# Kernel optimization log

Measured on AMD Instinct MI355X. Metric: run time of the kernel, lower is better.

The kernel has to match this reference:

```python
import jax, jax.numpy as jnp
import numpy as np

B, S, D, E, F, TOP_K = 4, 2048, 1024, 8, 4096, 2

def setup_inputs() -> dict:
    key = jax.random.key(0)
    ks = jax.random.split(key, 7)
    sd = 1.0 / np.sqrt(D)
    sf = 1.0 / np.sqrt(F)
    return {
        "x": jax.random.normal(ks[0], (B, S, D), dtype=jnp.float32),
        "gate_w": jax.random.normal(ks[1], (D, E), dtype=jnp.float32) * sd,
        "gate_b": jnp.zeros((E,), dtype=jnp.float32),
        "w1": jax.random.normal(ks[2], (E, D, F), dtype=jnp.float32) * sd,
        "b1": jnp.zeros((E, F), dtype=jnp.float32),
        "w2": jax.random.normal(ks[3], (E, F, D), dtype=jnp.float32) * sf,
        "b2": jnp.zeros((E, D), dtype=jnp.float32),
    }

def reference(x, gate_w, gate_b, w1, b1, w2, b2):
    # Gating: softmax over experts, take top-k, renormalize top-k weights.
    logits = jnp.einsum("bsd,de->bse", x, gate_w) + gate_b
    probs = jax.nn.softmax(logits, axis=-1)
    topw, topi = jax.lax.top_k(probs, TOP_K)            # [B,S,K]
    topw = topw / jnp.sum(topw, axis=-1, keepdims=True)
    # Sparse combine weights as dense [B,S,E] (zero for non-selected experts).
    combine = jnp.sum(jax.nn.one_hot(topi, E, dtype=x.dtype) * topw[..., None], axis=-2)  # [B,S,E]
    # Expert FFN (Linear -> ReLU -> Linear) computed for all experts, combined sparsely.
    mid = jax.nn.relu(jnp.einsum("bsd,edf->bsef", x, w1) + b1)   # [B,S,E,F]
    out_e = jnp.einsum("bsef,efd->bsed", mid, w2) + b2           # [B,S,E,D]
    return jnp.einsum("bsed,bse->bsd", out_e, combine)
```

## Files before the change

kernel.cpp:

```cpp
#include <hip/hip_runtime.h>

#define B_ 4
#define S_ 2048
#define T_ (B_*S_)
#define D_ 1024
#define E_ 8
#define F_ 4096
#define K_ 2
#define TK_ (T_*K_)

typedef __attribute__((ext_vector_type(8))) short short8;
typedef __attribute__((ext_vector_type(4))) float f32x4;

__device__ __forceinline__ unsigned short bf16rn(float f) {
    unsigned int u = __builtin_bit_cast(unsigned int, f);
    u = u + 0x7FFFu + ((u >> 16) & 1u);
    return (unsigned short)(u >> 16);
}
__device__ __forceinline__ float bf16tof(unsigned short h) {
    unsigned int u = ((unsigned int)h) << 16;
    return __builtin_bit_cast(float, u);
}

#define GLOAD16(gp, lp) __builtin_amdgcn_global_load_lds( \
    (const __attribute__((address_space(1))) unsigned int*)(gp), \
    (__attribute__((address_space(3))) unsigned int*)(lp), 16, 0, 0)

__global__ void gate_kernel(const float* __restrict__ x, const float* __restrict__ gw,
                            const float* __restrict__ gb, int* __restrict__ topi,
                            float* __restrict__ topw, int* __restrict__ counts)
{
    const int gid  = blockIdx.x * blockDim.x + threadIdx.x;
    const int t    = gid >> 6;
    const int lane = threadIdx.x & 63;
    if (t >= T_) return;
    const float* xr = x + (size_t)t * D_;
    float p[E_];
#pragma unroll
    for (int e = 0; e < E_; ++e) p[e] = 0.f;
    for (int j = 0; j < D_ / 64; ++j) {
        const int d = j * 64 + lane;
        const float xv = xr[d];
        const float* g = gw + (size_t)d * E_;
#pragma unroll
        for (int e = 0; e < E_; ++e) p[e] += xv * g[e];
    }
#pragma unroll
    for (int off = 32; off > 0; off >>= 1) {
#pragma unroll
        for (int e = 0; e < E_; ++e) p[e] += __shfl_xor(p[e], off);
    }
    if (lane == 0) {
#pragma unroll
        for (int e = 0; e < E_; ++e) p[e] += gb[e];
        float m = p[0];
#pragma unroll
        for (int e = 1; e < E_; ++e) m = fmaxf(m, p[e]);
        float ex[E_];
#pragma unroll
        for (int e = 0; e < E_; ++e) ex[e] = expf(p[e] - m);
        int i0 = 0; float v0 = ex[0];
#pragma unroll
        for (int e = 1; e < E_; ++e) if (ex[e] > v0) { v0 = ex[e]; i0 = e; }
        int i1 = -1; float v1 = -1.f;
#pragma unroll
        for (int e = 0; e < E_; ++e) if (e != i0 && ex[e] > v1) { v1 = ex[e]; i1 = e; }
        const float inv = 1.f / (v0 + v1);
        topi[t*2]   = i0; topi[t*2+1] = i1;
        topw[t*2]   = v0 * inv; topw[t*2+1] = v1 * inv;
        atomicAdd(&counts[i0], 1);
        atomicAdd(&counts[i1], 1);
    }
}

__global__ void offsets_kernel(const int* __restrict__ counts, int* __restrict__ offsets,
                               int* __restrict__ cursor)
{
    if (threadIdx.x == 0 && blockIdx.x == 0) {
        int acc = 0;
        for (int e = 0; e < E_; ++e) { offsets[e] = acc; cursor[e] = acc; acc += counts[e]; }
    }
}

__global__ void scatter_kernel(const int* __restrict__ topi, const float* __restrict__ topw,
                               int* __restrict__ cursor, int* __restrict__ list_token,
                               float* __restrict__ list_w, int* __restrict__ slot_of)
{
    const int t = blockIdx.x * blockDim.x + threadIdx.x;
    if (t >= T_) return;
#pragma unroll
    for (int k = 0; k < K_; ++k) {
        const int e = topi[t*2 + k];
        const int s = atomicAdd(&cursor[e], 1);
        list_token[s] = t;
        list_w[s]     = topw[t*2 + k];
        slot_of[t*2 + k] = s;
    }
}

__global__ void convert_x_kernel(const float* __restrict__ x,
                                 unsigned short* __restrict__ xh,
                                 unsigned short* __restrict__ xl)
{
    const size_t i = (size_t)blockIdx.x * blockDim.x + threadIdx.x;
    const float4 v = ((const float4*)x)[i];
    ushort4 h, l;
    h.x = bf16rn(v.x); l.x = bf16rn(v.x - bf16tof(h.x));
    h.y = bf16rn(v.y); l.y = bf16rn(v.y - bf16tof(h.y));
    h.z = bf16rn(v.z); l.z = bf16rn(v.z - bf16tof(h.z));
    h.w = bf16rn(v.w); l.w = bf16rn(v.w - bf16tof(h.w));
    ((ushort4*)xh)[i] = h;
    ((ushort4*)xl)[i] = l;
}

__global__ __launch_bounds__(256) void tconv_kernel(const float* __restrict__ in,
                                                    unsigned short* __restrict__ oh,
                                                    unsigned short* __restrict__ ol,
                                                    int R, int C)
{
    const int e = blockIdx.z;
    const size_t eb = (size_t)e * R * C;
    const int c0 = blockIdx.x * 32, r0 = blockIdx.y * 32;
    __shared__ float t[32][33];
    const int tx = threadIdx.x & 31, ty = threadIdx.x >> 5;
#pragma unroll
    for (int p = 0; p < 4; ++p)
        t[ty + 8*p][tx] = in[eb + (size_t)(r0 + ty + 8*p) * C + c0 + tx];
    __syncthreads();
#pragma unroll
    for (int p = 0; p < 4; ++p) {
        const float v = t[tx][ty + 8*p];
        const unsigned short h = bf16rn(v);
        const unsigned short lo = bf16rn(v - bf16tof(h));
        const size_t o = eb + (size_t)(c0 + ty + 8*p) * R + r0 + tx;
        oh[o] = h; ol[o] = lo;
    }
}

__global__ __launch_bounds__(256, 2) void gemm1_mfma(
    const unsigned short* __restrict__ xh, const unsigned short* __restrict__ xl,
    const unsigned short* __restrict__ w1h, const unsigned short* __restrict__ w1l,
    const float* __restrict__ b1,
    const int* __restrict__ list_token, const int* __restrict__ offsets,
    const int* __restrict__ counts,
    unsigned short* __restrict__ midh, unsigned short* __restrict__ midl,
    int f0, int Fc)
{
    const int e   = blockIdx.z;
    const int cnt = counts[e];
    const int r0  = blockIdx.x * 128;
    if (r0 >= cnt) return;
    const int base = offsets[e];
    const int fcol = f0 + blockIdx.y * 128;

    __shared__ unsigned short lds[4 * 4096];

    const int tid = threadIdx.x;
    const int w = tid >> 6, l = tid & 63;

    const unsigned short* gsrc[8];
    {
        const unsigned short* Abase = (w == 0) ? xh : xl;
        const unsigned short* Bbase = (w == 2) ? w1h : w1l;
        const int jr = l >> 2, pos = l & 3;
#pragma unroll
        for (int j = 0; j < 8; ++j) {
            const int r  = j * 16 + jr;
            const int kg = pos ^ ((r >> 1) & 3);
            if (w < 2) {
                int idx = base + r0 + r; if (idx > TK_ - 1) idx = TK_ - 1;
                const int tok = list_token[idx];
                gsrc[j] = Abase + (size_t)tok * D_ + kg * 8;
            } else {
                gsrc[j] = Bbase + ((size_t)e * F_ + fcol + r) * D_ + kg * 8;
            }
        }
    }
    unsigned short* ldst[8];
#pragma unroll
    for (int j = 0; j < 8; ++j) ldst[j] = &lds[w * 4096 + j * 512];

    const int wr = w >> 1, wc = w & 1;
    int idxA[4], idxB[4];
#pragma unroll
    for (int m = 0; m < 4; ++m) {
        const int row = wr * 64 + m * 16 + (l & 15);
        const int kgr = (l >> 4) ^ ((row >> 1) & 3);
        idxA[m] = row * 32 + kgr * 8;
    }
#pragma unroll
    for (int n = 0; n < 4; ++n) {
        const int row = wc * 64 + n * 16 + (l & 15);
        const int kgr = (l >> 4) ^ ((row >> 1) & 3);
        idxB[n] = row * 32 + kgr * 8;
    }

    f32x4 acc[4][4];
#pragma unroll
    for (int m = 0; m < 4; ++m)
#pragma unroll
        for (int n = 0; n < 4; ++n) { f32x4 z = {0.f,0.f,0.f,0.f}; acc[m][n] = z; }

    for (int k0 = 0; k0 < D_; k0 += 32) {
#pragma unroll
        for (int j = 0; j < 8; ++j) GLOAD16(gsrc[j] + k0, ldst[j]);
        __syncthreads();
        short8 ah[4], al[4], bh[4], bl[4];
#pragma unroll
        for (int m = 0; m < 4; ++m) {
            ah[m] = *(const short8*)&lds[0 * 4096 + idxA[m]];
            al[m] = *(const short8*)&lds[1 * 4096 + idxA[m]];
        }
#pragma unroll
        for (int n = 0; n < 4; ++n) {
            bh[n] = *(const short8*)&lds[2 * 4096 + idxB[n]];
            bl[n] = *(const short8*)&lds[3 * 4096 + idxB[n]];
        }
#pragma unroll
        for (int m = 0; m < 4; ++m)
#pragma unroll
            for (int n = 0; n < 4; ++n) {
                acc[m][n] = __builtin_amdgcn_mfma_f32_16x16x32_bf16(ah[m], bh[n], acc[m][n], 0, 0, 0);
                acc[m][n] = __builtin_amdgcn_mfma_f32_16x16x32_bf16(ah[m], bl[n], acc[m][n], 0, 0, 0);
                acc[m][n] = __builtin_amdgcn_mfma_f32_16x16x32_bf16(al[m], bh[n], acc[m][n], 0, 0, 0);
            }
        __syncthreads();
    }

    const float* b1e = b1 + (size_t)e * F_;
#pragma unroll
    for (int n = 0; n < 4; ++n) {
        const int fg = fcol + wc * 64 + n * 16 + (l & 15);
        const float bias = b1e[fg];
        const int fl = fg - f0;
#pragma unroll
        for (int m = 0; m < 4; ++m)
#pragma unroll
            for (int q = 0; q < 4; ++q) {
                const int rr = r0 + wr * 64 + m * 16 + (l >> 4) * 4 + q;
                if (rr < cnt) {
                    float v = acc[m][n][q] + bias;
                    v = fmaxf(v, 0.f);
                    const unsigned short h = bf16rn(v);
                    const unsigned short lo = bf16rn(v - bf16tof(h));
                    const size_t o = (size_t)(base + rr) * Fc + fl;
                    midh[o] = h; midl[o] = lo;
                }
            }
    }
}

__global__ __launch_bounds__(256, 2) void gemm2_mfma(
    const unsigned short* __restrict__ midh, const unsigned short* __restrict__ midl,
    const unsigned short* __restrict__ w2h, const unsigned short* __restrict__ w2l,
    const float* __restrict__ b2, const float* __restrict__ list_w,
    const int* __restrict__ offsets, const int* __restrict__ counts,
    float* __restrict__ part, int f0, int Fc, int first)
{
    const int e   = blockIdx.z;
    const int cnt = counts[e];
    const int r0  = blockIdx.x * 128;
    if (r0 >= cnt) return;
    const int base = offsets[e];
    const int dcol = blockIdx.y * 128;

    __shared__ unsigned short lds[4 * 4096];

    const int tid = threadIdx.x;
    const int w = tid >> 6, l = tid & 63;

    const unsigned short* gsrc[8];
    {
        const unsigned short* Abase = (w == 0) ? midh : midl;
        const unsigned short* Bbase = (w == 2) ? w2h : w2l;
        const int jr = l >> 2, pos = l & 3;
#pragma unroll
        for (int j = 0; j < 8; ++j) {
            const int r  = j * 16 + jr;
            const int kg = pos ^ ((r >> 1) & 3);
            if (w < 2) {
                int slot = base + r0 + r; if (slot > TK_ - 1) slot = TK_ - 1;
                gsrc[j] = Abase + (size_t)slot * Fc + kg * 8;
            } else {
                gsrc[j] = Bbase + ((size_t)e * D_ + dcol + r) * F_ + f0 + kg * 8;
            }
        }
    }
    unsigned short* ldst[8];
#pragma unroll
    for (int j = 0; j < 8; ++j) ldst[j] = &lds[w * 4096 + j * 512];

    const int wr = w >> 1, wc = w & 1;
    int idxA[4], idxB[4];
#pragma unroll
    for (int m = 0; m < 4; ++m) {
        const int row = wr * 64 + m * 16 + (l & 15);
        const int kgr = (l >> 4) ^ ((row >> 1) & 3);
        idxA[m] = row * 32 + kgr * 8;
    }
#pragma unroll
    for (int n = 0; n < 4; ++n) {
        const int row = wc * 64 + n * 16 + (l & 15);
        const int kgr = (l >> 4) ^ ((row >> 1) & 3);
        idxB[n] = row * 32 + kgr * 8;
    }

    f32x4 acc[4][4];
#pragma unroll
    for (int m = 0; m < 4; ++m)
#pragma unroll
        for (int n = 0; n < 4; ++n) { f32x4 z = {0.f,0.f,0.f,0.f}; acc[m][n] = z; }

    for (int k0 = 0; k0 < Fc; k0 += 32) {
#pragma unroll
        for (int j = 0; j < 8; ++j) GLOAD16(gsrc[j] + k0, ldst[j]);
        __syncthreads();
        short8 ah[4], al[4], bh[4], bl[4];
#pragma unroll
        for (int m = 0; m < 4; ++m) {
            ah[m] = *(const short8*)&lds[0 * 4096 + idxA[m]];
            al[m] = *(const short8*)&lds[1 * 4096 + idxA[m]];
        }
#pragma unroll
        for (int n = 0; n < 4; ++n) {
            bh[n] = *(const short8*)&lds[2 * 4096 + idxB[n]];
            bl[n] = *(const short8*)&lds[3 * 4096 + idxB[n]];
        }
#pragma unroll
        for (int m = 0; m < 4; ++m)
#pragma unroll
            for (int n = 0; n < 4; ++n) {
                acc[m][n] = __builtin_amdgcn_mfma_f32_16x16x32_bf16(ah[m], bh[n], acc[m][n], 0, 0, 0);
                acc[m][n] = __builtin_amdgcn_mfma_f32_16x16x32_bf16(ah[m], bl[n], acc[m][n], 0, 0, 0);
                acc[m][n] = __builtin_amdgcn_mfma_f32_16x16x32_bf16(al[m], bh[n], acc[m][n], 0, 0, 0);
            }
        __syncthreads();
    }

    float bias[4]; int dg[4];
#pragma unroll
    for (int n = 0; n < 4; ++n) {
        dg[n] = dcol + wc * 64 + n * 16 + (l & 15);
        bias[n] = b2[(size_t)e * D_ + dg[n]];
    }
#pragma unroll
    for (int m = 0; m < 4; ++m)
#pragma unroll
        for (int q = 0; q < 4; ++q) {
            const int rr = r0 + wr * 64 + m * 16 + (l >> 4) * 4 + q;
            if (rr < cnt) {
                const size_t s = (size_t)(base + rr);
                const float lw = list_w[s];
#pragma unroll
                for (int n = 0; n < 4; ++n) {
                    float v = acc[m][n][q] * lw;
                    if (first) v += lw * bias[n];
                    const size_t o = s * D_ + dg[n];
                    part[o] = first ? v : (part[o] + v);
                }
            }
        }
}

__global__ void combine_kernel(const float* __restrict__ part, const int* __restrict__ slot_of,
                               float* __restrict__ out)
{
    const int idx = blockIdx.x * blockDim.x + threadIdx.x;
    const int t  = idx >> 8;
    const int dq = idx & 255;
    const float4* p4 = (const float4*)part;
    const float4 a = p4[(size_t)slot_of[t*2]   * 256 + dq];
    const float4 b = p4[(size_t)slot_of[t*2+1] * 256 + dq];
    float4 r; r.x = a.x + b.x; r.y = a.y + b.y; r.z = a.z + b.z; r.w = a.w + b.w;
    ((float4*)out)[(size_t)t * 256 + dq] = r;
}

#define TILE 128
#define KSTEP 8
__global__ __launch_bounds__(256) void gemm1_f32(
    const float* __restrict__ x, const float* __restrict__ w1, const float* __restrict__ b1,
    const int* __restrict__ list_token, const int* __restrict__ offsets,
    const int* __restrict__ counts, float* __restrict__ mid, int f0, int Fc)
{
    const int e   = blockIdx.z;
    const int cnt = counts[e];
    const int r0  = blockIdx.x * TILE;
    if (r0 >= cnt) return;
    const int base = offsets[e];
    const int fcol = f0 + blockIdx.y * TILE;
    const int tid  = threadIdx.x;
    __shared__ float As[KSTEP][TILE + 4];
    __shared__ float Bs[KSTEP][TILE + 4];
    const int arow = tid >> 1;
    const int akq  = (tid & 1) * 4;
    const float* aptr = nullptr;
    if (r0 + arow < cnt) aptr = x + (size_t)list_token[base + r0 + arow] * D_;
    const int brow = tid >> 5;
    const int bcol = (tid & 31) * 4;
    const float* bptr = w1 + ((size_t)e * D_ + brow) * F_ + fcol + bcol;
    const int mb = (tid >> 4) * 8, nb = (tid & 15) * 8;
    float acc[8][8];
#pragma unroll
    for (int i = 0; i < 8; ++i)
#pragma unroll
        for (int j = 0; j < 8; ++j) acc[i][j] = 0.f;
    for (int k0 = 0; k0 < D_; k0 += KSTEP) {
        const float4 av = aptr ? *(const float4*)(aptr + k0 + akq) : make_float4(0.f,0.f,0.f,0.f);
        const float4 bv = *(const float4*)(bptr + (size_t)k0 * F_);
        __syncthreads();
        As[akq+0][arow] = av.x; As[akq+1][arow] = av.y;
        As[akq+2][arow] = av.z; As[akq+3][arow] = av.w;
        *(float4*)&Bs[brow][bcol] = bv;
        __syncthreads();
#pragma unroll
        for (int kk = 0; kk < KSTEP; ++kk) {
            const float4 a0 = *(const float4*)&As[kk][mb];
            const float4 a1 = *(const float4*)&As[kk][mb+4];
            const float4 b0 = *(const float4*)&Bs[kk][nb];
            const float4 b1v = *(const float4*)&Bs[kk][nb+4];
            const float af[8] = {a0.x,a0.y,a0.z,a0.w,a1.x,a1.y,a1.z,a1.w};
            const float bf[8] = {b0.x,b0.y,b0.z,b0.w,b1v.x,b1v.y,b1v.z,b1v.w};
#pragma unroll
            for (int i = 0; i < 8; ++i)
#pragma unroll
                for (int j = 0; j < 8; ++j) acc[i][j] = fmaf(af[i], bf[j], acc[i][j]);
        }
    }
    const int fc_local = fcol - f0;
#pragma unroll
    for (int i = 0; i < 8; ++i) {
        const int r = r0 + mb + i;
        if (r < cnt) {
            const size_t s = (size_t)(base + r);
            const size_t off = s * (size_t)Fc + fc_local + nb;
#pragma unroll
            for (int j = 0; j < 8; ++j) {
                const float v = acc[i][j] + b1[(size_t)e * F_ + fcol + nb + j];
                mid[off + j] = fmaxf(v, 0.f);
            }
        }
    }
}

__global__ __launch_bounds__(256) void gemm2_f32(
    const float* __restrict__ mid, const float* __restrict__ w2, const float* __restrict__ b2,
    const float* __restrict__ list_w, const int* __restrict__ offsets,
    const int* __restrict__ counts, float* __restrict__ part, int f0, int Fc, int first)
{
    const int e   = blockIdx.z;
    const int cnt = counts[e];
    const int r0  = blockIdx.x * TILE;
    if (r0 >= cnt) return;
    const int base = offsets[e];
    const int dcol = blockIdx.y * TILE;
    const int tid  = threadIdx.x;
    __shared__ float As[KSTEP][TILE + 4];
    __shared__ float Bs[KSTEP][TILE + 4];
    const int arow = tid >> 1;
    const int akq  = (tid & 1) * 4;
    const float* aptr = nullptr;
    if (r0 + arow < cnt) aptr = mid + (size_t)(base + r0 + arow) * Fc;
    const int brow = tid >> 5;
    const int bcol = (tid & 31) * 4;
    const float* bptr = w2 + ((size_t)e * F_ + f0 + brow) * D_ + dcol + bcol;
    const int mb = (tid >> 4) * 8, nb = (tid & 15) * 8;
    float acc[8][8];
#pragma unroll
    for (int i = 0; i < 8; ++i)
#pragma unroll
        for (int j = 0; j < 8; ++j) acc[i][j] = 0.f;
    for (int k0 = 0; k0 < Fc; k0 += KSTEP) {
        const float4 av = aptr ? *(const float4*)(aptr + k0 + akq) : make_float4(0.f,0.f,0.f,0.f);
        const float4 bv = *(const float4*)(bptr + (size_t)k0 * D_);
        __syncthreads();
        As[akq+0][arow] = av.x; As[akq+1][arow] = av.y;
        As[akq+2][arow] = av.z; As[akq+3][arow] = av.w;
        *(float4*)&Bs[brow][bcol] = bv;
        __syncthreads();
#pragma unroll
        for (int kk = 0; kk < KSTEP; ++kk) {
            const float4 a0 = *(const float4*)&As[kk][mb];
            const float4 a1 = *(const float4*)&As[kk][mb+4];
            const float4 b0 = *(const float4*)&Bs[kk][nb];
            const float4 b1v = *(const float4*)&Bs[kk][nb+4];
            const float af[8] = {a0.x,a0.y,a0.z,a0.w,a1.x,a1.y,a1.z,a1.w};
            const float bf[8] = {b0.x,b0.y,b0.z,b0.w,b1v.x,b1v.y,b1v.z,b1v.w};
#pragma unroll
            for (int i = 0; i < 8; ++i)
#pragma unroll
                for (int j = 0; j < 8; ++j) acc[i][j] = fmaf(af[i], bf[j], acc[i][j]);
        }
    }
#pragma unroll
    for (int i = 0; i < 8; ++i) {
        const int r = r0 + mb + i;
        if (r < cnt) {
            const size_t s = (size_t)(base + r);
            const float lw = list_w[s];
            const size_t po = s * (size_t)D_ + dcol + nb;
#pragma unroll
            for (int j = 0; j < 8; ++j) {
                float v = acc[i][j] * lw;
                if (first) v += lw * b2[(size_t)e * D_ + dcol + nb + j];
                part[po + j] = first ? v : (part[po + j] + v);
            }
        }
    }
}

extern "C" void kernel_launch(void* const* d_in, const int* in_sizes, int n_in,
                              void* d_out, int out_size, void* d_ws, size_t ws_size,
                              hipStream_t stream)
{
    (void)in_sizes; (void)n_in; (void)out_size;
    const float* x      = (const float*)d_in[0];
    const float* gate_w = (const float*)d_in[1];
    const float* gate_b = (const float*)d_in[2];
    const float* w1     = (const float*)d_in[3];
    const float* b1     = (const float*)d_in[4];
    const float* w2     = (const float*)d_in[5];
    const float* b2     = (const float*)d_in[6];
    float* out = (float*)d_out;
    char*  ws  = (char*)d_ws;

    size_t off = 0;
    auto alloc = [&](size_t bytes) { size_t o = off; off = (off + bytes + 255) & ~255ULL; return o; };
    const size_t o_counts = alloc(64);
    const size_t o_cursor = alloc(64);
    const size_t o_offs   = alloc(64);
    const size_t o_topi   = alloc((size_t)TK_ * 4);
    const size_t o_topw   = alloc((size_t)TK_ * 4);
    const size_t o_slot   = alloc((size_t)TK_ * 4);
    const size_t o_ltok   = alloc((size_t)(TK_ + 256) * 4);
    const size_t o_lw     = alloc((size_t)TK_ * 4);
    const size_t o_part   = alloc((size_t)TK_ * D_ * 4);
    const size_t o_xh     = alloc((size_t)T_ * D_ * 2);
    const size_t o_xl     = alloc((size_t)T_ * D_ * 2);
    const size_t o_w1h    = alloc((size_t)E_ * D_ * F_ * 2);
    const size_t o_w1l    = alloc((size_t)E_ * D_ * F_ * 2);
    const size_t o_w2h    = alloc((size_t)E_ * D_ * F_ * 2);
    const size_t o_w2l    = alloc((size_t)E_ * D_ * F_ * 2);
    const size_t fixed = off;

    int*   counts     = (int*)(ws + o_counts);
    int*   cursor     = (int*)(ws + o_cursor);
    int*   offsets    = (int*)(ws + o_offs);
    int*   topi       = (int*)(ws + o_topi);
    float* topw       = (float*)(ws + o_topw);
    int*   slot_of    = (int*)(ws + o_slot);
    int*   list_token = (int*)(ws + o_ltok);
    float* list_w     = (float*)(ws + o_lw);
    float* part       = (float*)(ws + o_part);

    hipMemsetAsync(counts, 0, 64, stream);
    gate_kernel<<<T_/4, 256, 0, stream>>>(x, gate_w, gate_b, topi, topw, counts);
    offsets_kernel<<<1, 64, 0, stream>>>(counts, offsets, cursor);
    scatter_kernel<<<T_/256, 256, 0, stream>>>(topi, topw, cursor, list_token, list_w, slot_of);

    const bool mfma_ok = fixed + (size_t)TK_ * 128 * 2 * 2 + 512 <= ws_size;
    if (mfma_ok) {
        int Fc = F_;
        while (Fc > 128 && fixed + (size_t)TK_ * Fc * 2 * 2 + 512 > ws_size) Fc >>= 1;
        unsigned short* xh   = (unsigned short*)(ws + o_xh);
        unsigned short* xl   = (unsigned short*)(ws + o_xl);
        unsigned short* w1h  = (unsigned short*)(ws + o_w1h);
        unsigned short* w1l  = (unsigned short*)(ws + o_w1l);
        unsigned short* w2h  = (unsigned short*)(ws + o_w2h);
        unsigned short* w2l  = (unsigned short*)(ws + o_w2l);
        unsigned short* midh = (unsigned short*)(ws + fixed);
        unsigned short* midl = midh + (size_t)TK_ * Fc;

        convert_x_kernel<<<(T_*D_/4)/256, 256, 0, stream>>>(x, xh, xl);
        tconv_kernel<<<dim3(F_/32, D_/32, E_), 256, 0, stream>>>(w1, w1h, w1l, D_, F_);
        tconv_kernel<<<dim3(D_/32, F_/32, E_), 256, 0, stream>>>(w2, w2h, w2l, F_, D_);

        const int NC = F_ / Fc;
        for (int c = 0; c < NC; ++c) {
            gemm1_mfma<<<dim3(TK_/128, Fc/128, E_), 256, 0, stream>>>(
                xh, xl, w1h, w1l, b1, list_token, offsets, counts, midh, midl, c*Fc, Fc);
            gemm2_mfma<<<dim3(TK_/128, D_/128, E_), 256, 0, stream>>>(
                midh, midl, w2h, w2l, b2, list_w, offsets, counts, part, c*Fc, Fc, c == 0);
        }
    } else {
        float* mid = (float*)(ws + o_xh);
        size_t avail = (ws_size > o_xh) ? ws_size - o_xh : 0;
        int Fc = 1024;
        while (Fc > 128 && (size_t)TK_ * Fc * 4 > avail) Fc >>= 1;
        const int NC = F_ / Fc;
        for (int c = 0; c < NC; ++c) {
            gemm1_f32<<<dim3(TK_/TILE, Fc/TILE, E_), 256, 0, stream>>>(
                x, w1, b1, list_token, offsets, counts, mid, c*Fc, Fc);
            gemm2_f32<<<dim3(TK_/TILE, D_/TILE, E_), 256, 0, stream>>>(
                mid, w2, b2, list_w, offsets, counts, part, c*Fc, Fc, c == 0);
        }
    }
    combine_kernel<<<(T_*D_/4)/256, 256, 0, stream>>>(part, slot_of, out);
}
```

Measured before the change: 2.272 ms.

## Double-buffer LDS tiles in expert GEMMs and vectorize weight transpose-convert

Both MFMA GEMM kernels now use two LDS buffers: the next K-tile's global-to-LDS loads are issued right after the barrier, while the current tile is being consumed. This removes one barrier per iteration and aims to hide load latency behind the MFMA work. LDS use per block doubles to 64 KB, which may limit occupancy at the requested two blocks per CU. The weight transpose-convert kernel also switches from an LDS 32x32 tile to a register 4x4 transpose per thread. It uses float4 reads and ushort4 writes over 64x64 blocks, aiming to raise memory throughput.

```diff
diff --git a/kernel.cpp b/kernel.cpp
--- a/kernel.cpp
+++ b/kernel.cpp
@@ -120,23 +120,28 @@
 {
     const int e = blockIdx.z;
     const size_t eb = (size_t)e * R * C;
-    const int c0 = blockIdx.x * 32, r0 = blockIdx.y * 32;
-    __shared__ float t[32][33];
-    const int tx = threadIdx.x & 31, ty = threadIdx.x >> 5;
-#pragma unroll
-    for (int p = 0; p < 4; ++p)
-        t[ty + 8*p][tx] = in[eb + (size_t)(r0 + ty + 8*p) * C + c0 + tx];
-    __syncthreads();
-#pragma unroll
-    for (int p = 0; p < 4; ++p) {
-        const float v = t[tx][ty + 8*p];
-        const unsigned short h = bf16rn(v);
-        const unsigned short lo = bf16rn(v - bf16tof(h));
-        const size_t o = eb + (size_t)(c0 + ty + 8*p) * R + r0 + tx;
-        oh[o] = h; ol[o] = lo;
-    }
-}
-
+    const int r4 = blockIdx.y * 64 + ((threadIdx.x >> 4) << 2);
+    const int c4 = blockIdx.x * 64 + ((threadIdx.x & 15) << 2);
+    float4 v[4];
+#pragma unroll
+    for (int i = 0; i < 4; ++i)
+        v[i] = *(const float4*)&in[eb + (size_t)(r4 + i) * C + c4];
+    const float* vf = (const float*)v;
+#pragma unroll
+    for (int j = 0; j < 4; ++j) {
+        ushort4 h, l;
+        float f;
+        f = vf[0*4+j]; h.x = bf16rn(f); l.x = bf16rn(f - bf16tof(h.x));
+        f = vf[1*4+j]; h.y = bf16rn(f); l.y = bf16rn(f - bf16tof(h.y));
+        f = vf[2*4+j]; h.z = bf16rn(f); l.z = bf16rn(f - bf16tof(h.z));
+        f = vf[3*4+j]; h.w = bf16rn(f); l.w = bf16rn(f - bf16tof(h.w));
+        const size_t o = eb + (size_t)(c4 + j) * R + r4;
+        *(ushort4*)&oh[o] = h;
+        *(ushort4*)&ol[o] = l;
+    }
+}
+
+#define PLANE4 (4*4096)
 __global__ __launch_bounds__(256, 2) void gemm1_mfma(
     const unsigned short* __restrict__ xh, const unsigned short* __restrict__ xl,
     const unsigned short* __restrict__ w1h, const unsigned short* __restrict__ w1l,
@@ -153,7 +158,7 @@
     const int base = offsets[e];
     const int fcol = f0 + blockIdx.y * 128;
 
-    __shared__ unsigned short lds[4 * 4096];
+    __shared__ unsigned short lds[2 * PLANE4];
 
     const int tid = threadIdx.x;
     const int w = tid >> 6, l = tid & 63;
@@ -176,9 +181,6 @@
             }
         }
     }
-    unsigned short* ldst[8];
-#pragma unroll
-    for (int j = 0; j < 8; ++j) ldst[j] = &lds[w * 4096 + j * 512];
 
     const int wr = w >> 1, wc = w & 1;
     int idxA[4], idxB[4];
@@ -201,20 +203,31 @@
 #pragma unroll
         for (int n = 0; n < 4; ++n) { f32x4 z = {0.f,0.f,0.f,0.f}; acc[m][n] = z; }
 
-    for (int k0 = 0; k0 < D_; k0 += 32) {
-#pragma unroll
-        for (int j = 0; j < 8; ++j) GLOAD16(gsrc[j] + k0, ldst[j]);
+    const int NK = D_ / 32;
+    {
+        unsigned short* dst = &lds[w * 4096];
+#pragma unroll
+        for (int j = 0; j < 8; ++j) GLOAD16(gsrc[j], dst + j * 512);
+    }
+    for (int kt = 0; kt < NK; ++kt) {
         __syncthreads();
+        if (kt + 1 < NK) {
+            unsigned short* dst = &lds[((kt + 1) & 1) * PLANE4 + w * 4096];
+            const int koff = (kt + 1) * 32;
+#pragma unroll
+            for (int j = 0; j < 8; ++j) GLOAD16(gsrc[j] + koff, dst + j * 512);
+        }
+        const unsigned short* cur = &lds[(kt & 1) * PLANE4];
         short8 ah[4], al[4], bh[4], bl[4];
 #pragma unroll
         for (int m = 0; m < 4; ++m) {
-            ah[m] = *(const short8*)&lds[0 * 4096 + idxA[m]];
-            al[m] = *(const short8*)&lds[1 * 4096 + idxA[m]];
+            ah[m] = *(const short8*)&cur[0 * 4096 + idxA[m]];
+            al[m] = *(const short8*)&cur[1 * 4096 + idxA[m]];
         }
 #pragma unroll
         for (int n = 0; n < 4; ++n) {
-            bh[n] = *(const short8*)&lds[2 * 4096 + idxB[n]];
-            bl[n] = *(const short8*)&lds[3 * 4096 + idxB[n]];
+            bh[n] = *(const short8*)&cur[2 * 4096 + idxB[n]];
+            bl[n] = *(const short8*)&cur[3 * 4096 + idxB[n]];
         }
 #pragma unroll
         for (int m = 0; m < 4; ++m)
@@ -224,7 +237,6 @@
                 acc[m][n] = __builtin_amdgcn_mfma_f32_16x16x32_bf16(ah[m], bl[n], acc[m][n], 0, 0, 0);
                 acc[m][n] = __builtin_amdgcn_mfma_f32_16x16x32_bf16(al[m], bh[n], acc[m][n], 0, 0, 0);
             }
-        __syncthreads();
     }
 
     const float* b1e = b1 + (size_t)e * F_;
@@ -264,7 +276,7 @@
     const int base = offsets[e];
     const int dcol = blockIdx.y * 128;
 
-    __shared__ unsigned short lds[4 * 4096];
+    __shared__ unsigned short lds[2 * PLANE4];
 
     const int tid = threadIdx.x;
     const int w = tid >> 6, l = tid & 63;
@@ -286,9 +298,6 @@
             }
         }
     }
-    unsigned short* ldst[8];
-#pragma unroll
-    for (int j = 0; j < 8; ++j) ldst[j] = &lds[w * 4096 + j * 512];
 
     const int wr = w >> 1, wc = w & 1;
     int idxA[4], idxB[4];
@@ -311,20 +320,31 @@
 #pragma unroll
         for (int n = 0; n < 4; ++n) { f32x4 z = {0.f,0.f,0.f,0.f}; acc[m][n] = z; }
 
-    for (int k0 = 0; k0 < Fc; k0 += 32) {
-#pragma unroll
-        for (int j = 0; j < 8; ++j) GLOAD16(gsrc[j] + k0, ldst[j]);
+    const int NK = Fc / 32;
+    {
+        unsigned short* dst = &lds[w * 4096];
+#pragma unroll
+        for (int j = 0; j < 8; ++j) GLOAD16(gsrc[j], dst + j * 512);
+    }
+    for (int kt = 0; kt < NK; ++kt) {
         __syncthreads();
+        if (kt + 1 < NK) {
+            unsigned short* dst = &lds[((kt + 1) & 1) * PLANE4 + w * 4096];
+            const int koff = (kt + 1) * 32;
+#pragma unroll
+            for (int j = 0; j < 8; ++j) GLOAD16(gsrc[j] + koff, dst + j * 512);
+        }
+        const unsigned short* cur = &lds[(kt & 1) * PLANE4];
         short8 ah[4], al[4], bh[4], bl[4];
 #pragma unroll
         for (int m = 0; m < 4; ++m) {
-            ah[m] = *(const short8*)&lds[0 * 4096 + idxA[m]];
-            al[m] = *(const short8*)&lds[1 * 4096 + idxA[m]];
+            ah[m] = *(const short8*)&cur[0 * 4096 + idxA[m]];
+            al[m] = *(const short8*)&cur[1 * 4096 + idxA[m]];
         }
 #pragma unroll
         for (int n = 0; n < 4; ++n) {
-            bh[n] = *(const short8*)&lds[2 * 4096 + idxB[n]];
-            bl[n] = *(const short8*)&lds[3 * 4096 + idxB[n]];
+            bh[n] = *(const short8*)&cur[2 * 4096 + idxB[n]];
+            bl[n] = *(const short8*)&cur[3 * 4096 + idxB[n]];
         }
 #pragma unroll
         for (int m = 0; m < 4; ++m)
@@ -334,7 +354,6 @@
                 acc[m][n] = __builtin_amdgcn_mfma_f32_16x16x32_bf16(ah[m], bl[n], acc[m][n], 0, 0, 0);
                 acc[m][n] = __builtin_amdgcn_mfma_f32_16x16x32_bf16(al[m], bh[n], acc[m][n], 0, 0, 0);
             }
-        __syncthreads();
     }
 
     float bias[4]; int dg[4];
@@ -571,8 +590,8 @@
         unsigned short* midl = midh + (size_t)TK_ * Fc;
 
         convert_x_kernel<<<(T_*D_/4)/256, 256, 0, stream>>>(x, xh, xl);
-        tconv_kernel<<<dim3(F_/32, D_/32, E_), 256, 0, stream>>>(w1, w1h, w1l, D_, F_);
-        tconv_kernel<<<dim3(D_/32, F_/32, E_), 256, 0, stream>>>(w2, w2h, w2l, F_, D_);
+        tconv_kernel<<<dim3(F_/64, D_/64, E_), 256, 0, stream>>>(w1, w1h, w1l, D_, F_);
+        tconv_kernel<<<dim3(D_/64, F_/64, E_), 256, 0, stream>>>(w2, w2h, w2l, F_, D_);
 
         const int NC = F_ / Fc;
         for (int c = 0; c < NC; ++c) {
```

New measurement: 2.438 ms. 1.07x slower.
